# Performance work log

Hardware: AMD Instinct MI355X
Metric: run time of the kernel (lower is better)

## Reference

```python
import jax, jax.numpy as jnp
import numpy as np

B, T, C = 2, 2048, 1024
NUM_HEADS = 16
HEAD_DIM = C // NUM_HEADS
TEMP = 1.0
LN_EPS = 1e-6


def setup_inputs() -> dict:
    key = jax.random.key(0)
    kx, kqw, kpw = jax.random.split(key, 3)
    x = jax.random.normal(kx, (B, T, C), dtype=jnp.float32)
    # causal mask, broadcastable to [B, H, T, T]
    mask = jnp.tril(jnp.ones((T, T), dtype=bool))[None, None, :, :]
    # LayerNorm params (flax defaults: scale=1, bias=0)
    ln_scale = jnp.ones((C,), dtype=jnp.float32)
    ln_bias = jnp.zeros((C,), dtype=jnp.float32)
    # xavier_uniform init for dense kernels, zero bias (torch_linear)
    lim_qkv = float(np.sqrt(6.0 / (C + 3 * C)))
    qkv_w = jax.random.uniform(kqw, (C, 3 * C), jnp.float32, -lim_qkv, lim_qkv)
    qkv_b = jnp.zeros((3 * C,), dtype=jnp.float32)
    lim_p = float(np.sqrt(6.0 / (C + C)))
    proj_w = jax.random.uniform(kpw, (C, C), jnp.float32, -lim_p, lim_p)
    proj_b = jnp.zeros((C,), dtype=jnp.float32)
    return {"x": x, "mask": mask, "ln_scale": ln_scale, "ln_bias": ln_bias,
            "qkv_w": qkv_w, "qkv_b": qkv_b, "proj_w": proj_w, "proj_b": proj_b}


def reference(x, mask, ln_scale, ln_bias, qkv_w, qkv_b, proj_w, proj_b):
    b, t, c = x.shape
    # LayerNorm (eps=1e-6, flax default)
    mu = jnp.mean(x, axis=-1, keepdims=True)
    var = jnp.mean(jnp.square(x - mu), axis=-1, keepdims=True)
    xn = (x - mu) * jax.lax.rsqrt(var + LN_EPS) * ln_scale + ln_bias
    # fused QKV projection
    qkv = xn @ qkv_w + qkv_b
    q, k, v = jnp.split(qkv, 3, axis=-1)
    q = q.reshape(b, t, NUM_HEADS, HEAD_DIM) / TEMP
    k = k.reshape(b, t, NUM_HEADS, HEAD_DIM)
    v = v.reshape(b, t, NUM_HEADS, HEAD_DIM)
    # scaled dot-product attention with mask (eval path: no dropout)
    q = q / jnp.sqrt(jnp.float32(HEAD_DIM)).astype(x.dtype)
    scores = jnp.einsum('bqhd,bkhd->bhqk', q, k)  # [B,H,T,T]
    big_neg = jnp.finfo(x.dtype).min
    scores = jnp.where(mask, scores, big_neg)
    attn_weights = jax.nn.softmax(scores, axis=-1).astype(x.dtype)
    out = jnp.einsum('bhqk,bkhd->bqhd', attn_weights, v).reshape(b, t, c)
    return out @ proj_w + proj_b
```

## Files before the change

kernel.cpp:

```cpp
#include <hip/hip_runtime.h>
#include <cstdint>
#include <math.h>

#define DEV __device__ __forceinline__

typedef unsigned int u32;
typedef unsigned short u16;
typedef __attribute__((ext_vector_type(4))) float f32x4;
typedef __attribute__((ext_vector_type(4))) u32 u32x4;
typedef __attribute__((ext_vector_type(2))) u32 u32x2;
typedef __attribute__((ext_vector_type(8))) __bf16 bf16x8;

static_assert(sizeof(bf16x8) == 16, "bf16x8 must be 16B");

static constexpr int Tn = 2048, Cn = 1024;
static constexpr float QSCALE2 = 0.125f * 1.44269504088896f;

DEV u16 f2bf_rne(float f) {
  u32 u = __builtin_bit_cast(u32, f);
  u32 r = u + 0x7fffu + ((u >> 16) & 1u);
  return (u16)(r >> 16);
}
DEV float bf2f(u16 h) {
  u32 u = ((u32)h) << 16;
  return __builtin_bit_cast(float, u);
}
DEV u32 pack2bf(float a, float b) {
  return (u32)f2bf_rne(a) | ((u32)f2bf_rne(b) << 16);
}
DEV float fexp2(float x) {
#if __has_builtin(__builtin_amdgcn_exp2f)
  return __builtin_amdgcn_exp2f(x);
#else
  return exp2f(x);
#endif
}

DEV void stage16(const void* g, void* l) {
#if __has_builtin(__builtin_amdgcn_global_load_lds)
  __builtin_amdgcn_global_load_lds(
      (__attribute__((address_space(1))) u32*)(uintptr_t)g,
      (__attribute__((address_space(3))) u32*)l, 16, 0, 0);
#else
  *(u32x4*)l = *(const u32x4*)g;
#endif
}

__global__ __launch_bounds__(256) void pre_kernel(const float* __restrict__ x,
                                                  const float* __restrict__ sc,
                                                  const float* __restrict__ bi,
                                                  u16* __restrict__ xn,
                                                  const float* __restrict__ qkv_w,
                                                  u16* __restrict__ wqkv,
                                                  const float* __restrict__ proj_w,
                                                  u16* __restrict__ wproj) {
  __shared__ float shm[32 * 33];
  int t = threadIdx.x;
  if (blockIdx.x < 4096) {
    int row = blockIdx.x;
    const float* xr = x + (size_t)row * Cn;
    f32x4 v = *(const f32x4*)(xr + t * 4);
    float s = v.x + v.y + v.z + v.w;
    float s2 = v.x * v.x + v.y * v.y + v.z * v.z + v.w * v.w;
#pragma unroll
    for (int off = 1; off < 64; off <<= 1) {
      s += __shfl_xor(s, off);
      s2 += __shfl_xor(s2, off);
    }
    if ((t & 63) == 0) {
      shm[(t >> 6) * 2] = s;
      shm[(t >> 6) * 2 + 1] = s2;
    }
    __syncthreads();
    s = shm[0] + shm[2] + shm[4] + shm[6];
    s2 = shm[1] + shm[3] + shm[5] + shm[7];
    float mean = s * (1.0f / Cn);
    float var = s2 * (1.0f / Cn) - mean * mean;
    float rstd = rsqrtf(var + 1e-6f);
    f32x4 g = *(const f32x4*)(sc + t * 4);
    f32x4 b = *(const f32x4*)(bi + t * 4);
    u32 lo = pack2bf((v.x - mean) * rstd * g.x + b.x, (v.y - mean) * rstd * g.y + b.y);
    u32 hi = pack2bf((v.z - mean) * rstd * g.z + b.z, (v.w - mean) * rstd * g.w + b.w);
    u32x2 pack = {lo, hi};
    *(u32x2*)(xn + (size_t)row * Cn + t * 4) = pack;
  } else {
    int idx = blockIdx.x - 4096;
    int bx = idx & 127, by = idx >> 7;
    const float* src;
    u16* dst;
    int Cc;
    if (bx < 96) {
      src = qkv_w; dst = wqkv; Cc = 3072;
    } else {
      src = proj_w; dst = wproj; Cc = 1024; bx -= 96;
    }
    int tx = t & 31, ty = t >> 5;
    int c0 = bx * 32, r0 = by * 32;
#pragma unroll
    for (int k = 0; k < 4; ++k)
      shm[(ty + 8 * k) * 33 + tx] = src[(size_t)(r0 + ty + 8 * k) * Cc + c0 + tx];
    __syncthreads();
#pragma unroll
    for (int k = 0; k < 4; ++k)
      dst[(size_t)(c0 + ty + 8 * k) * 1024 + r0 + tx] =
          f2bf_rne(shm[tx * 33 + ty + 8 * k]);
  }
}

template <bool OUT_F32, bool QKV>
__global__ __launch_bounds__(256, 3) void gemm_kernel(const u16* __restrict__ A,
                                                      const u16* __restrict__ Bt,
                                                      const float* __restrict__ bias,
                                                      void* __restrict__ Cout,
                                                      u16* __restrict__ vtp,
                                                      int Nsz, int Ksz) {
  __shared__ u16 As[128 * 64];
  __shared__ u16 Bs[128 * 64];
  int t = threadIdx.x;
  int l = t & 63, w = t >> 6;
  int quad = l >> 4, c16 = l & 15;
  int wm = w & 1, wn = w >> 1;
  int m0 = blockIdx.y * 128, n0 = blockIdx.x * 128;

  f32x4 acc[4][4];
#pragma unroll
  for (int mt = 0; mt < 4; ++mt)
#pragma unroll
    for (int nt = 0; nt < 4; ++nt) acc[mt][nt] = (f32x4){0.f, 0.f, 0.f, 0.f};

  for (int kk = 0; kk < Ksz; kk += 64) {
#pragma unroll
    for (int i = 0; i < 4; ++i) {
      int c = t + i * 256;
      int m = c >> 3, k8 = (c & 7) ^ (m & 7);
      stage16(A + (size_t)(m0 + m) * Ksz + kk + k8 * 8, (char*)As + c * 16);
    }
#pragma unroll
    for (int i = 0; i < 4; ++i) {
      int c = t + i * 256;
      int n = c >> 3, k8 = (c & 7) ^ (n & 7);
      stage16(Bt + (size_t)(n0 + n) * Ksz + kk + k8 * 8, (char*)Bs + c * 16);
    }
    __syncthreads();
#pragma unroll
    for (int h = 0; h < 2; ++h) {
      bf16x8 af[4], bf[4];
#pragma unroll
      for (int mt = 0; mt < 4; ++mt) {
        int m = wm * 64 + mt * 16 + c16;
        int LC = m * 8 + ((h * 4 + quad) ^ (m & 7));
        af[mt] = *(const bf16x8*)((const char*)As + LC * 16);
      }
#pragma unroll
      for (int nt = 0; nt < 4; ++nt) {
        int n = wn * 64 + nt * 16 + c16;
        int LC = n * 8 + ((h * 4 + quad) ^ (n & 7));
        bf[nt] = *(const bf16x8*)((const char*)Bs + LC * 16);
      }
#pragma unroll
      for (int mt = 0; mt < 4; ++mt)
#pragma unroll
        for (int nt = 0; nt < 4; ++nt)
          acc[mt][nt] = __builtin_amdgcn_mfma_f32_16x16x32_bf16(af[mt], bf[nt],
                                                                acc[mt][nt], 0, 0, 0);
    }
    __syncthreads();
  }
#pragma unroll
  for (int mt = 0; mt < 4; ++mt) {
    int row = m0 + wm * 64 + mt * 16 + quad * 4;
#pragma unroll
    for (int nt = 0; nt < 4; ++nt) {
      int col = n0 + wn * 64 + nt * 16 + c16;
      float bv = bias[col];
      if (QKV && col >= 2048) {
        int hd = col - 2048;
        int bb = row >> 11, tt = row & 2047;
        u32x2 pk = {pack2bf(acc[mt][nt][0] + bv, acc[mt][nt][1] + bv),
                    pack2bf(acc[mt][nt][2] + bv, acc[mt][nt][3] + bv)};
        *(u32x2*)(vtp + ((size_t)bb * 1024 + hd) * 2048 + tt) = pk;
      } else {
        float scale = (QKV && col < 1024) ? QSCALE2 : 1.0f;
#pragma unroll
        for (int r = 0; r < 4; ++r) {
          float v = (acc[mt][nt][r] + bv) * scale;
          if (OUT_F32)
            ((float*)Cout)[(size_t)(row + r) * Nsz + col] = v;
          else
            ((u16*)Cout)[(size_t)(row + r) * Nsz + col] = f2bf_rne(v);
        }
      }
    }
  }
}

__constant__ int4 chunk_tab[24] = {
    {15, 0, 8, 0}, {15, 8, 8, 1}, {14, 0, 8, 0}, {7, 0, 8, -1},
    {14, 8, 7, 1}, {13, 0, 7, 0}, {13, 7, 7, 1}, {12, 0, 7, 0}, {6, 0, 7, -1},
    {12, 7, 6, 1}, {11, 0, 6, 0}, {11, 6, 6, 1}, {10, 0, 6, 0}, {5, 0, 6, -1},
    {10, 6, 5, 1}, {9, 0, 5, 0}, {9, 5, 5, 1}, {8, 0, 5, 0}, {4, 0, 5, -1},
    {8, 5, 4, 1}, {3, 0, 4, -1},
    {2, 0, 3, -1},
    {1, 0, 2, -1},
    {0, 0, 1, -1}};

__global__ __launch_bounds__(256, 2) void flash_kernel(const u16* __restrict__ qkv,
                                                       const u16* __restrict__ vt,
                                                       u16* __restrict__ aout,
                                                       u16* __restrict__ Op,
                                                       float* __restrict__ ml) {
  int4 ck = chunk_tab[blockIdx.x >> 5];
  int bh = blockIdx.x & 31;
  int qt = ck.x, k0 = ck.y, kend = ck.y + ck.z, half = ck.w;
  int b = bh >> 4, h = bh & 15;
  int t = threadIdx.x, l = t & 63, w = t >> 6;
  int quad = l >> 4, c16 = l & 15;
  int q0 = qt * 128;
  const u16* __restrict__ vtb = vt + (size_t)bh * 64 * 2048;

  __shared__ u16 Ks[128 * 64];
  __shared__ u16 Vs[64 * 128];
  __shared__ u16 Ps[128 * 128];

  bf16x8 qf[2][2];
#pragma unroll
  for (int nt = 0; nt < 2; ++nt)
#pragma unroll
    for (int ks = 0; ks < 2; ++ks)
      qf[nt][ks] = *(const bf16x8*)(qkv +
          (size_t)(b * Tn + q0 + w * 32 + nt * 16 + c16) * 3072 +
          h * 64 + ks * 32 + quad * 8);

  float mrow[2] = {-1e30f, -1e30f};
  float lrow[2] = {0.f, 0.f};
  f32x4 o[2][4];
#pragma unroll
  for (int mq = 0; mq < 2; ++mq)
#pragma unroll
    for (int dt = 0; dt < 4; ++dt) o[mq][dt] = (f32x4){0.f, 0.f, 0.f, 0.f};

#pragma unroll
  for (int i = 0; i < 4; ++i) {
    int c = t + i * 256;
    int key = c >> 3, d8 = (c & 7) ^ (key & 7);
    stage16(qkv + (size_t)(b * Tn + k0 * 128 + key) * 3072 + Cn + h * 64 + d8 * 8,
            (char*)Ks + c * 16);
  }
#pragma unroll
  for (int i = 0; i < 4; ++i) {
    int c = t + i * 256;
    int d = c >> 4, k8 = (c & 15) ^ (d & 15);
    stage16(vtb + (size_t)d * 2048 + k0 * 128 + k8 * 8, (char*)Vs + c * 16);
  }

  for (int kt = k0; kt < kend; ++kt) {
    __syncthreads();

    bf16x8 vf[4][4];
#pragma unroll
    for (int ks = 0; ks < 4; ++ks)
#pragma unroll
      for (int dt = 0; dt < 4; ++dt) {
        int d = dt * 16 + c16;
        int vc = d * 16 + ((ks * 4 + quad) ^ (d & 15));
        vf[ks][dt] = *(const bf16x8*)((const char*)Vs + vc * 16);
      }

    f32x4 s[8][2];
#pragma unroll
    for (int mt = 0; mt < 8; ++mt)
#pragma unroll
      for (int nt = 0; nt < 2; ++nt) s[mt][nt] = (f32x4){0.f, 0.f, 0.f, 0.f};
#pragma unroll
    for (int mt = 0; mt < 8; ++mt) {
#pragma unroll
      for (int ks = 0; ks < 2; ++ks) {
        int key = mt * 16 + c16;
        int d8 = ks * 4 + quad;
        int LC = key * 8 + (d8 ^ (key & 7));
        bf16x8 kf = *(const bf16x8*)((const char*)Ks + LC * 16);
#pragma unroll
        for (int nt = 0; nt < 2; ++nt)
          s[mt][nt] = __builtin_amdgcn_mfma_f32_16x16x32_bf16(kf, qf[nt][ks],
                                                              s[mt][nt], 0, 0, 0);
      }
    }

    __syncthreads();

    if (kt + 1 < kend) {
#pragma unroll
      for (int i = 0; i < 4; ++i) {
        int c = t + i * 256;
        int key = c >> 3, d8 = (c & 7) ^ (key & 7);
        stage16(qkv + (size_t)(b * Tn + (kt + 1) * 128 + key) * 3072 + Cn +
                    h * 64 + d8 * 8,
                (char*)Ks + c * 16);
      }
#pragma unroll
      for (int i = 0; i < 4; ++i) {
        int c = t + i * 256;
        int d = c >> 4, k8 = (c & 15) ^ (d & 15);
        stage16(vtb + (size_t)d * 2048 + (kt + 1) * 128 + k8 * 8,
                (char*)Vs + c * 16);
      }
    }

    if (kt == qt) {
#pragma unroll
      for (int mt = 0; mt < 8; ++mt)
#pragma unroll
        for (int nt = 0; nt < 2; ++nt)
#pragma unroll
          for (int r = 0; r < 4; ++r) {
            int key = kt * 128 + mt * 16 + quad * 4 + r;
            int q = q0 + w * 32 + nt * 16 + c16;
            if (key > q) s[mt][nt][r] = -1e30f;
          }
    }
    float alph[2];
#pragma unroll
    for (int nt = 0; nt < 2; ++nt) {
      float rm = -1e30f;
#pragma unroll
      for (int mt = 0; mt < 8; ++mt)
#pragma unroll
        for (int r = 0; r < 4; ++r) rm = fmaxf(rm, s[mt][nt][r]);
      rm = fmaxf(rm, __shfl_xor(rm, 16));
      rm = fmaxf(rm, __shfl_xor(rm, 32));
      float mnew = fmaxf(mrow[nt], rm);
      alph[nt] = fexp2(mrow[nt] - mnew);
      mrow[nt] = mnew;
      float rs = 0.f;
#pragma unroll
      for (int mt = 0; mt < 8; ++mt)
#pragma unroll
        for (int r = 0; r < 4; ++r) {
          float e = fexp2(s[mt][nt][r] - mnew);
          s[mt][nt][r] = e;
          rs += e;
        }
      rs += __shfl_xor(rs, 16);
      rs += __shfl_xor(rs, 32);
      lrow[nt] = lrow[nt] * alph[nt] + rs;
    }
#pragma unroll
    for (int mq = 0; mq < 2; ++mq)
#pragma unroll
      for (int r = 0; r < 4; ++r) {
        float a = __shfl(alph[mq], quad * 4 + r);
#pragma unroll
        for (int dt = 0; dt < 4; ++dt) o[mq][dt][r] *= a;
      }
#pragma unroll
    for (int mt = 0; mt < 8; ++mt)
#pragma unroll
      for (int nt = 0; nt < 2; ++nt) {
        int q = w * 32 + nt * 16 + c16;
        int kc = mt * 4 + quad;
        int LC = q * 32 + (kc ^ ((q & 15) << 1));
        u32x2 pk = {pack2bf(s[mt][nt][0], s[mt][nt][1]),
                    pack2bf(s[mt][nt][2], s[mt][nt][3])};
        *(u32x2*)((char*)Ps + LC * 8) = pk;
      }
#pragma unroll
    for (int ks = 0; ks < 4; ++ks) {
      bf16x8 pa[2];
#pragma unroll
      for (int mq = 0; mq < 2; ++mq) {
        int q = w * 32 + mq * 16 + c16;
        int kc = ks * 8 + quad * 2;
        int LC = q * 32 + (kc ^ ((q & 15) << 1));
        pa[mq] = *(const bf16x8*)((const char*)Ps + LC * 8);
      }
#pragma unroll
      for (int dt = 0; dt < 4; ++dt)
#pragma unroll
        for (int mq = 0; mq < 2; ++mq)
          o[mq][dt] = __builtin_amdgcn_mfma_f32_16x16x32_bf16(pa[mq], vf[ks][dt],
                                                              o[mq][dt], 0, 0, 0);
    }
  }

  float linv[2] = {1.0f / lrow[0], 1.0f / lrow[1]};
  if (half < 0) {
#pragma unroll
    for (int mq = 0; mq < 2; ++mq)
#pragma unroll
      for (int r = 0; r < 4; ++r) {
        float li = __shfl(linv[mq], quad * 4 + r);
        int q = q0 + w * 32 + mq * 16 + quad * 4 + r;
#pragma unroll
        for (int dt = 0; dt < 4; ++dt)
          aout[(size_t)(b * Tn + q) * 1024 + h * 64 + dt * 16 + c16] =
              f2bf_rne(o[mq][dt][r] * li);
      }
  } else {
    int ps = ((qt - 8) * 32 + bh) * 2 + half;
#pragma unroll
    for (int mq = 0; mq < 2; ++mq)
#pragma unroll
      for (int r = 0; r < 4; ++r) {
        float li = __shfl(linv[mq], quad * 4 + r);
        int qr = w * 32 + mq * 16 + quad * 4 + r;
#pragma unroll
        for (int dt = 0; dt < 4; ++dt)
          Op[((size_t)ps * 128 + qr) * 64 + dt * 16 + c16] =
              f2bf_rne(o[mq][dt][r] * li);
      }
    if (quad == 0) {
#pragma unroll
      for (int nt = 0; nt < 2; ++nt) {
        int qr = w * 32 + nt * 16 + c16;
        ml[((size_t)ps * 128 + qr) * 2] = mrow[nt];
        ml[((size_t)ps * 128 + qr) * 2 + 1] = lrow[nt];
      }
    }
  }
}

__global__ __launch_bounds__(256) void combine_kernel(const u16* __restrict__ Op,
                                                      const float* __restrict__ ml,
                                                      u16* __restrict__ aout) {
  int qt = 8 + (blockIdx.x >> 5);
  int bh = blockIdx.x & 31;
  int b = bh >> 4, h = bh & 15;
  int ps0 = ((qt - 8) * 32 + bh) * 2;
  int d = threadIdx.x & 63, rq = threadIdx.x >> 6;
  for (int r = 0; r < 32; ++r) {
    int row = rq * 32 + r;
    float m0 = ml[((size_t)ps0 * 128 + row) * 2];
    float l0 = ml[((size_t)ps0 * 128 + row) * 2 + 1];
    float m1 = ml[((size_t)(ps0 + 1) * 128 + row) * 2];
    float l1 = ml[((size_t)(ps0 + 1) * 128 + row) * 2 + 1];
    float M = fmaxf(m0, m1);
    float w0 = fexp2(m0 - M) * l0, w1 = fexp2(m1 - M) * l1;
    float inv = 1.0f / (w0 + w1);
    float o0 = bf2f(Op[((size_t)ps0 * 128 + row) * 64 + d]);
    float o1 = bf2f(Op[((size_t)(ps0 + 1) * 128 + row) * 64 + d]);
    aout[(size_t)(b * Tn + qt * 128 + row) * 1024 + h * 64 + d] =
        f2bf_rne((w0 * o0 + w1 * o1) * inv);
  }
}

extern "C" void kernel_launch(void* const* d_in, const int* in_sizes, int n_in,
                              void* d_out, int out_size, void* d_ws, size_t ws_size,
                              hipStream_t stream) {
  const float* x = (const float*)d_in[0];
  const float* ln_s = (const float*)d_in[2];
  const float* ln_b = (const float*)d_in[3];
  const float* qkv_w = (const float*)d_in[4];
  const float* qkv_b = (const float*)d_in[5];
  const float* proj_w = (const float*)d_in[6];
  const float* proj_b = (const float*)d_in[7];
  float* out = (float*)d_out;
  char* ws = (char*)d_ws;

  u16* xn = (u16*)ws;
  u16* wqkv = (u16*)(ws + (8ull << 20));
  u16* wproj = (u16*)(ws + (14ull << 20));
  u16* qkvm = (u16*)(ws + (16ull << 20));
  u16* attn = (u16*)(ws + (40ull << 20));
  u16* vt = (u16*)(ws + (48ull << 20));
  u16* Op = (u16*)ws;
  float* ml = (float*)(ws + (8ull << 20));

  pre_kernel<<<8192, 256, 0, stream>>>(x, ln_s, ln_b, xn, qkv_w, wqkv, proj_w,
                                       wproj);
  gemm_kernel<false, true><<<dim3(24, 32), 256, 0, stream>>>(xn, wqkv, qkv_b, qkvm,
                                                             vt, 3072, 1024);
  flash_kernel<<<768, 256, 0, stream>>>(qkvm, vt, attn, Op, ml);
  combine_kernel<<<256, 256, 0, stream>>>(Op, ml, attn);
  gemm_kernel<true, false><<<dim3(8, 32), 256, 0, stream>>>(attn, wproj, proj_b, out,
                                                            nullptr, 1024, 1024);
}
```

Before: 223.2 us.

## Double-buffer QKV GEMM with 256x128 tiles and restructure flash K/V staging

Splits the templated GEMM into two kernels. The QKV projection now uses a 256x128 tile with K-step 32, double-buffered shared memory, and a prefetch of the next K slice issued before the current MFMAs. The projection GEMM moves to K-step 32 with a new swizzle and stays single-buffered. In the flash kernel, the next-tile K/V prefetch overlap is removed in favour of load-then-sync each iteration, and V fragments are read from LDS inside the PV loop rather than hoisted, which lowers register pressure but serialises loads with compute.

New measurement: 222.2 us. No clear change (-0.5%).

```diff
diff --git a/kernel.cpp b/kernel.cpp
--- a/kernel.cpp
+++ b/kernel.cpp
@@ -107,89 +107,164 @@
   }
 }
 
-template <bool OUT_F32, bool QKV>
-__global__ __launch_bounds__(256, 3) void gemm_kernel(const u16* __restrict__ A,
-                                                      const u16* __restrict__ Bt,
-                                                      const float* __restrict__ bias,
-                                                      void* __restrict__ Cout,
-                                                      u16* __restrict__ vtp,
-                                                      int Nsz, int Ksz) {
-  __shared__ u16 As[128 * 64];
-  __shared__ u16 Bs[128 * 64];
+__global__ __launch_bounds__(256, 2) void gemm_qkv(const u16* __restrict__ A,
+                                                   const u16* __restrict__ Bt,
+                                                   const float* __restrict__ bias,
+                                                   u16* __restrict__ qkvm,
+                                                   u16* __restrict__ vtp) {
+  __shared__ u16 As[2][256 * 32];
+  __shared__ u16 Bs[2][128 * 32];
   int t = threadIdx.x;
   int l = t & 63, w = t >> 6;
   int quad = l >> 4, c16 = l & 15;
-  int wm = w & 1, wn = w >> 1;
-  int m0 = blockIdx.y * 128, n0 = blockIdx.x * 128;
-
-  f32x4 acc[4][4];
+  int m0 = blockIdx.y * 256, n0 = blockIdx.x * 128;
+
+  f32x4 acc[4][8];
 #pragma unroll
   for (int mt = 0; mt < 4; ++mt)
 #pragma unroll
-    for (int nt = 0; nt < 4; ++nt) acc[mt][nt] = (f32x4){0.f, 0.f, 0.f, 0.f};
-
-  for (int kk = 0; kk < Ksz; kk += 64) {
-#pragma unroll
-    for (int i = 0; i < 4; ++i) {
-      int c = t + i * 256;
-      int m = c >> 3, k8 = (c & 7) ^ (m & 7);
-      stage16(A + (size_t)(m0 + m) * Ksz + kk + k8 * 8, (char*)As + c * 16);
-    }
-#pragma unroll
-    for (int i = 0; i < 4; ++i) {
-      int c = t + i * 256;
-      int n = c >> 3, k8 = (c & 7) ^ (n & 7);
-      stage16(Bt + (size_t)(n0 + n) * Ksz + kk + k8 * 8, (char*)Bs + c * 16);
-    }
-    __syncthreads();
-#pragma unroll
-    for (int h = 0; h < 2; ++h) {
-      bf16x8 af[4], bf[4];
-#pragma unroll
-      for (int mt = 0; mt < 4; ++mt) {
-        int m = wm * 64 + mt * 16 + c16;
-        int LC = m * 8 + ((h * 4 + quad) ^ (m & 7));
-        af[mt] = *(const bf16x8*)((const char*)As + LC * 16);
-      }
-#pragma unroll
-      for (int nt = 0; nt < 4; ++nt) {
-        int n = wn * 64 + nt * 16 + c16;
-        int LC = n * 8 + ((h * 4 + quad) ^ (n & 7));
-        bf[nt] = *(const bf16x8*)((const char*)Bs + LC * 16);
-      }
-#pragma unroll
-      for (int mt = 0; mt < 4; ++mt)
-#pragma unroll
-        for (int nt = 0; nt < 4; ++nt)
-          acc[mt][nt] = __builtin_amdgcn_mfma_f32_16x16x32_bf16(af[mt], bf[nt],
-                                                                acc[mt][nt], 0, 0, 0);
-    }
-    __syncthreads();
+    for (int nt = 0; nt < 8; ++nt) acc[mt][nt] = (f32x4){0.f, 0.f, 0.f, 0.f};
+
+#pragma unroll
+  for (int i = 0; i < 4; ++i) {
+    int c = t + i * 256;
+    int m = c >> 2, k8 = (c & 3) ^ ((m >> 1) & 3);
+    stage16(A + (size_t)(m0 + m) * 1024 + k8 * 8, (char*)As[0] + c * 16);
+  }
+#pragma unroll
+  for (int i = 0; i < 2; ++i) {
+    int c = t + i * 256;
+    int n = c >> 2, k8 = (c & 3) ^ ((n >> 1) & 3);
+    stage16(Bt + (size_t)(n0 + n) * 1024 + k8 * 8, (char*)Bs[0] + c * 16);
+  }
+
+  for (int ki = 0; ki < 32; ++ki) {
+    int p = ki & 1;
+    __syncthreads();
+    if (ki + 1 < 32) {
+      int kk = (ki + 1) * 32;
+#pragma unroll
+      for (int i = 0; i < 4; ++i) {
+        int c = t + i * 256;
+        int m = c >> 2, k8 = (c & 3) ^ ((m >> 1) & 3);
+        stage16(A + (size_t)(m0 + m) * 1024 + kk + k8 * 8,
+                (char*)As[p ^ 1] + c * 16);
+      }
+#pragma unroll
+      for (int i = 0; i < 2; ++i) {
+        int c = t + i * 256;
+        int n = c >> 2, k8 = (c & 3) ^ ((n >> 1) & 3);
+        stage16(Bt + (size_t)(n0 + n) * 1024 + kk + k8 * 8,
+                (char*)Bs[p ^ 1] + c * 16);
+      }
+    }
+    bf16x8 af[4], bf[8];
+#pragma unroll
+    for (int mt = 0; mt < 4; ++mt) {
+      int m = w * 64 + mt * 16 + c16;
+      int LC = m * 4 + (quad ^ ((m >> 1) & 3));
+      af[mt] = *(const bf16x8*)((const char*)As[p] + LC * 16);
+    }
+#pragma unroll
+    for (int nt = 0; nt < 8; ++nt) {
+      int n = nt * 16 + c16;
+      int LC = n * 4 + (quad ^ ((n >> 1) & 3));
+      bf[nt] = *(const bf16x8*)((const char*)Bs[p] + LC * 16);
+    }
+#pragma unroll
+    for (int mt = 0; mt < 4; ++mt)
+#pragma unroll
+      for (int nt = 0; nt < 8; ++nt)
+        acc[mt][nt] = __builtin_amdgcn_mfma_f32_16x16x32_bf16(af[mt], bf[nt],
+                                                              acc[mt][nt], 0, 0, 0);
   }
 #pragma unroll
   for (int mt = 0; mt < 4; ++mt) {
-    int row = m0 + wm * 64 + mt * 16 + quad * 4;
-#pragma unroll
-    for (int nt = 0; nt < 4; ++nt) {
-      int col = n0 + wn * 64 + nt * 16 + c16;
+    int row = m0 + w * 64 + mt * 16 + quad * 4;
+#pragma unroll
+    for (int nt = 0; nt < 8; ++nt) {
+      int col = n0 + nt * 16 + c16;
       float bv = bias[col];
-      if (QKV && col >= 2048) {
+      if (col >= 2048) {
         int hd = col - 2048;
         int bb = row >> 11, tt = row & 2047;
         u32x2 pk = {pack2bf(acc[mt][nt][0] + bv, acc[mt][nt][1] + bv),
                     pack2bf(acc[mt][nt][2] + bv, acc[mt][nt][3] + bv)};
         *(u32x2*)(vtp + ((size_t)bb * 1024 + hd) * 2048 + tt) = pk;
       } else {
-        float scale = (QKV && col < 1024) ? QSCALE2 : 1.0f;
-#pragma unroll
-        for (int r = 0; r < 4; ++r) {
-          float v = (acc[mt][nt][r] + bv) * scale;
-          if (OUT_F32)
-            ((float*)Cout)[(size_t)(row + r) * Nsz + col] = v;
-          else
-            ((u16*)Cout)[(size_t)(row + r) * Nsz + col] = f2bf_rne(v);
-        }
-      }
+        float scale = (col < 1024) ? QSCALE2 : 1.0f;
+#pragma unroll
+        for (int r = 0; r < 4; ++r)
+          qkvm[(size_t)(row + r) * 3072 + col] = f2bf_rne((acc[mt][nt][r] + bv) * scale);
+      }
+    }
+  }
+}
+
+__global__ __launch_bounds__(256, 3) void gemm_proj(const u16* __restrict__ A,
+                                                    const u16* __restrict__ Bt,
+                                                    const float* __restrict__ bias,
+                                                    float* __restrict__ Cout,
+                                                    int Nsz, int Ksz) {
+  __shared__ u16 As[128 * 32];
+  __shared__ u16 Bs[128 * 32];
+  int t = threadIdx.x;
+  int l = t & 63, w = t >> 6;
+  int quad = l >> 4, c16 = l & 15;
+  int wm = w & 1, wn = w >> 1;
+  int m0 = blockIdx.y * 128, n0 = blockIdx.x * 128;
+
+  f32x4 acc[4][4];
+#pragma unroll
+  for (int mt = 0; mt < 4; ++mt)
+#pragma unroll
+    for (int nt = 0; nt < 4; ++nt) acc[mt][nt] = (f32x4){0.f, 0.f, 0.f, 0.f};
+
+  for (int kk = 0; kk < Ksz; kk += 32) {
+#pragma unroll
+    for (int i = 0; i < 2; ++i) {
+      int c = t + i * 256;
+      int m = c >> 2, k8 = (c & 3) ^ ((m >> 1) & 3);
+      stage16(A + (size_t)(m0 + m) * Ksz + kk + k8 * 8, (char*)As + c * 16);
+    }
+#pragma unroll
+    for (int i = 0; i < 2; ++i) {
+      int c = t + i * 256;
+      int n = c >> 2, k8 = (c & 3) ^ ((n >> 1) & 3);
+      stage16(Bt + (size_t)(n0 + n) * Ksz + kk + k8 * 8, (char*)Bs + c * 16);
+    }
+    __syncthreads();
+    bf16x8 af[4], bf[4];
+#pragma unroll
+    for (int mt = 0; mt < 4; ++mt) {
+      int m = wm * 64 + mt * 16 + c16;
+      int LC = m * 4 + (quad ^ ((m >> 1) & 3));
+      af[mt] = *(const bf16x8*)((const char*)As + LC * 16);
+    }
+#pragma unroll
+    for (int nt = 0; nt < 4; ++nt) {
+      int n = wn * 64 + nt * 16 + c16;
+      int LC = n * 4 + (quad ^ ((n >> 1) & 3));
+      bf[nt] = *(const bf16x8*)((const char*)Bs + LC * 16);
+    }
+#pragma unroll
+    for (int mt = 0; mt < 4; ++mt)
+#pragma unroll
+      for (int nt = 0; nt < 4; ++nt)
+        acc[mt][nt] = __builtin_amdgcn_mfma_f32_16x16x32_bf16(af[mt], bf[nt],
+                                                              acc[mt][nt], 0, 0, 0);
+    __syncthreads();
+  }
+#pragma unroll
+  for (int mt = 0; mt < 4; ++mt) {
+    int row = m0 + wm * 64 + mt * 16 + quad * 4;
+#pragma unroll
+    for (int nt = 0; nt < 4; ++nt) {
+      int col = n0 + wn * 64 + nt * 16 + c16;
+      float bv = bias[col];
+#pragma unroll
+      for (int r = 0; r < 4; ++r)
+        Cout[(size_t)(row + r) * Nsz + col] = acc[mt][nt][r] + bv;
     }
   }
 }
@@ -239,32 +314,21 @@
 #pragma unroll
     for (int dt = 0; dt < 4; ++dt) o[mq][dt] = (f32x4){0.f, 0.f, 0.f, 0.f};
 
-#pragma unroll
-  for (int i = 0; i < 4; ++i) {
-    int c = t + i * 256;
-    int key = c >> 3, d8 = (c & 7) ^ (key & 7);
-    stage16(qkv + (size_t)(b * Tn + k0 * 128 + key) * 3072 + Cn + h * 64 + d8 * 8,
-            (char*)Ks + c * 16);
-  }
-#pragma unroll
-  for (int i = 0; i < 4; ++i) {
-    int c = t + i * 256;
-    int d = c >> 4, k8 = (c & 15) ^ (d & 15);
-    stage16(vtb + (size_t)d * 2048 + k0 * 128 + k8 * 8, (char*)Vs + c * 16);
-  }
-
   for (int kt = k0; kt < kend; ++kt) {
-    __syncthreads();
-
-    bf16x8 vf[4][4];
-#pragma unroll
-    for (int ks = 0; ks < 4; ++ks)
-#pragma unroll
-      for (int dt = 0; dt < 4; ++dt) {
-        int d = dt * 16 + c16;
-        int vc = d * 16 + ((ks * 4 + quad) ^ (d & 15));
-        vf[ks][dt] = *(const bf16x8*)((const char*)Vs + vc * 16);
-      }
+#pragma unroll
+    for (int i = 0; i < 4; ++i) {
+      int c = t + i * 256;
+      int key = c >> 3, d8 = (c & 7) ^ (key & 7);
+      stage16(qkv + (size_t)(b * Tn + kt * 128 + key) * 3072 + Cn + h * 64 + d8 * 8,
+              (char*)Ks + c * 16);
+    }
+#pragma unroll
+    for (int i = 0; i < 4; ++i) {
+      int c = t + i * 256;
+      int d = c >> 4, k8 = (c & 15) ^ (d & 15);
+      stage16(vtb + (size_t)d * 2048 + kt * 128 + k8 * 8, (char*)Vs + c * 16);
+    }
+    __syncthreads();
 
     f32x4 s[8][2];
 #pragma unroll
@@ -285,27 +349,6 @@
                                                               s[mt][nt], 0, 0, 0);
       }
     }
-
-    __syncthreads();
-
-    if (kt + 1 < kend) {
-#pragma unroll
-      for (int i = 0; i < 4; ++i) {
-        int c = t + i * 256;
-        int key = c >> 3, d8 = (c & 7) ^ (key & 7);
-        stage16(qkv + (size_t)(b * Tn + (kt + 1) * 128 + key) * 3072 + Cn +
-                    h * 64 + d8 * 8,
-                (char*)Ks + c * 16);
-      }
-#pragma unroll
-      for (int i = 0; i < 4; ++i) {
-        int c = t + i * 256;
-        int d = c >> 4, k8 = (c & 15) ^ (d & 15);
-        stage16(vtb + (size_t)d * 2048 + (kt + 1) * 128 + k8 * 8,
-                (char*)Vs + c * 16);
-      }
-    }
-
     if (kt == qt) {
 #pragma unroll
       for (int mt = 0; mt < 8; ++mt)
@@ -374,12 +417,17 @@
         pa[mq] = *(const bf16x8*)((const char*)Ps + LC * 8);
       }
 #pragma unroll
-      for (int dt = 0; dt < 4; ++dt)
+      for (int dt = 0; dt < 4; ++dt) {
+        int d = dt * 16 + c16;
+        int vc = d * 16 + ((ks * 4 + quad) ^ (d & 15));
+        bf16x8 vf = *(const bf16x8*)((const char*)Vs + vc * 16);
 #pragma unroll
         for (int mq = 0; mq < 2; ++mq)
-          o[mq][dt] = __builtin_amdgcn_mfma_f32_16x16x32_bf16(pa[mq], vf[ks][dt],
-                                                              o[mq][dt], 0, 0, 0);
-    }
+          o[mq][dt] = __builtin_amdgcn_mfma_f32_16x16x32_bf16(pa[mq], vf, o[mq][dt],
+                                                              0, 0, 0);
+      }
+    }
+    __syncthreads();
   }
 
   float linv[2] = {1.0f / lrow[0], 1.0f / lrow[1]};
@@ -467,10 +515,8 @@
 
   pre_kernel<<<8192, 256, 0, stream>>>(x, ln_s, ln_b, xn, qkv_w, wqkv, proj_w,
                                        wproj);
-  gemm_kernel<false, true><<<dim3(24, 32), 256, 0, stream>>>(xn, wqkv, qkv_b, qkvm,
-                                                             vt, 3072, 1024);
+  gemm_qkv<<<dim3(24, 16), 256, 0, stream>>>(xn, wqkv, qkv_b, qkvm, vt);
   flash_kernel<<<768, 256, 0, stream>>>(qkvm, vt, attn, Op, ml);
   combine_kernel<<<256, 256, 0, stream>>>(Op, ml, attn);
-  gemm_kernel<true, false><<<dim3(8, 32), 256, 0, stream>>>(attn, wproj, proj_b, out,
-                                                            nullptr, 1024, 1024);
-}
+  gemm_proj<<<dim3(8, 32), 256, 0, stream>>>(attn, wproj, proj_b, out, 1024, 1024);
+}
```
